# Optimization experiments

Measured on AMD Instinct MI355X. Metric: run time of the kernel, lower is better.

## Reference

```python
import jax, jax.numpy as jnp
import numpy as np

N_NODES = 100000
N_EDGES = 640000
D = 128
L = 3


def setup_inputs() -> dict:
    key = jax.random.key(0)
    k1, k2, k3 = jax.random.split(key, 3)
    x = jax.random.normal(k1, (N_NODES, D), dtype=jnp.float32)
    edge_index = jax.random.randint(k2, (2, N_EDGES), 0, N_NODES, dtype=jnp.int64)
    batch = jnp.zeros((N_NODES,), dtype=jnp.int64)
    W = jax.random.normal(k3, (L, D, D), dtype=jnp.float32) / np.sqrt(D)
    b = jnp.zeros((L, D), dtype=jnp.float32)
    return {"x": x, "edge_index": edge_index, "batch": batch, "W": W, "b": b}


def _gcn_forward(x, edge_index, W, b):
    row, col = edge_index[0], edge_index[1]  # source, target
    n = x.shape[0]
    # symmetric normalization (PyG gcn_norm, add_self_loops=False, unit edge weights)
    deg = jax.ops.segment_sum(jnp.ones((row.shape[0],), dtype=x.dtype), col, num_segments=n)
    dinv = jnp.where(deg > 0, jax.lax.rsqrt(jnp.where(deg > 0, deg, 1.0)), 0.0)
    norm = dinv[row] * dinv[col]  # [E]
    for i in range(W.shape[0]):
        h = x @ W[i]                                   # [N, D]
        msg = h[row] * norm[:, None]                   # gather + scale, [E, D]
        x = jax.ops.segment_sum(msg, col, num_segments=n) + b[i]
        if i < W.shape[0] - 1:
            x = jax.nn.relu(x)
    return x


def reference(x, edge_index, batch, W, b):
    return _gcn_forward(x, edge_index, W, b)
```

## Files before the change

kernel.cpp:

```cpp
#include <hip/hip_runtime.h>
#include <hip/hip_fp16.h>
#include <math.h>

#define NN 100000
#define NE 640000
#define DD 128
#define LSTRIDE 132
#define SLOT_CAP 32

typedef __attribute__((ext_vector_type(8))) short short8;
typedef __attribute__((ext_vector_type(4))) float floatx4;

#define EPI_PRE_F32 0
#define EPI_PRE_F16 1
#define EPI_FINAL   2

static const size_t OFF_DEG    = 0;
static const size_t OFF_GCTR   = 400000;
static const size_t OFF_DINV   = 400064;
static const size_t OFF_OFF    = 800064;
static const size_t OFF_CURSOR = 1200064;
static const size_t OFF_WHP    = 1600064;
static const size_t OFF_WLP    = 1698368;
static const size_t OFF_EIDX   = 1796672;
static const size_t OFF_H_FB   = 4357120;
static const size_t WS_NEED_FB = 4357120 + (size_t)NN * DD * 4;
static const size_t OFF_SLOT   = 1796672;
static const size_t OFF_X16    = 14596672;
static const size_t OFF_ZA     = 40196928;
static const size_t WS_NEED_SL = 40196928 + (size_t)(NN + 1) * DD * 2;

__device__ __forceinline__ unsigned bf16_rne(float f) {
    unsigned u = __float_as_uint(f);
    return (u + 0x7FFFu + ((u >> 16) & 1u)) >> 16;
}

__device__ __forceinline__ void pack_W(int t, const float* __restrict__ W,
                                       ushort* __restrict__ Whp,
                                       ushort* __restrict__ Wlp) {
    if (t < 3 * 2048) {
        int l = t >> 11;
        int r = t & 2047;
        int kc = r >> 9;
        int nt = (r >> 6) & 7;
        int L  = r & 63;
        int n  = nt * 16 + (L & 15);
        int k0 = kc * 32 + (L >> 4) * 8;
        const float* Wl_ = W + (size_t)l * DD * DD;
        size_t base = ((size_t)l * 2048 + r) * 8;
        #pragma unroll
        for (int j = 0; j < 8; ++j) {
            float f = Wl_[(size_t)(k0 + j) * DD + n];
            unsigned hi = bf16_rne(f);
            float fh = __uint_as_float(hi << 16);
            unsigned lo = bf16_rne(f - fh);
            Whp[base + j] = (ushort)hi;
            Wlp[base + j] = (ushort)lo;
        }
    }
}

__global__ __launch_bounds__(256) void fill_slots_pack(const int* __restrict__ rowi,
                                                       const int* __restrict__ coli,
                                                       int* __restrict__ cnt,
                                                       int* __restrict__ slot,
                                                       const float* __restrict__ W,
                                                       ushort* __restrict__ Whp,
                                                       ushort* __restrict__ Wlp) {
    int t = blockIdx.x * 256 + threadIdx.x;
    int e0 = t * 4;
    if (e0 < NE) {
        int4 s4 = *(const int4*)(rowi + e0);
        int4 d4 = *(const int4*)(coli + e0);
        int p0 = atomicAdd(&cnt[d4.x], 1);
        int p1 = atomicAdd(&cnt[d4.y], 1);
        int p2 = atomicAdd(&cnt[d4.z], 1);
        int p3 = atomicAdd(&cnt[d4.w], 1);
        if (p0 < SLOT_CAP) slot[(d4.x << 5) + p0] = s4.x;
        if (p1 < SLOT_CAP) slot[(d4.y << 5) + p1] = s4.y;
        if (p2 < SLOT_CAP) slot[(d4.z << 5) + p2] = s4.z;
        if (p3 < SLOT_CAP) slot[(d4.w << 5) + p3] = s4.w;
    }
    pack_W(t, W, Whp, Wlp);
}

__global__ __launch_bounds__(256) void prescale_convert(const float* __restrict__ x,
                                                        int* __restrict__ cnt,
                                                        float* __restrict__ dinv,
                                                        __half* __restrict__ x16,
                                                        __half* __restrict__ za) {
    int t = blockIdx.x * 256 + threadIdx.x;
    int row = t >> 5;
    int c4  = (t & 31) * 4;
    int d = cnt[row];
    float s = (d > 0) ? 1.0f / sqrtf((float)d) : 0.0f;
    if ((t & 31) == 0) {
        if (d > SLOT_CAP) cnt[row] = SLOT_CAP;
        dinv[row] = s;
    }
    float4 v = *(const float4*)(x + (size_t)row * DD + c4);
    __half2 p0 = __floats2half2_rn(v.x * s, v.y * s);
    __half2 p1 = __floats2half2_rn(v.z * s, v.w * s);
    uint2 w;
    w.x = *(unsigned*)&p0;
    w.y = *(unsigned*)&p1;
    *(uint2*)(x16 + (size_t)row * DD + c4) = w;
    if (blockIdx.x == 0 && threadIdx.x < 128) {
        __half z = __float2half(0.f);
        x16[(size_t)NN * DD + threadIdx.x] = z;
        za [(size_t)NN * DD + threadIdx.x] = z;
    }
}

__global__ __launch_bounds__(256) void count_and_pack(const int* __restrict__ coli,
                                                      int* __restrict__ deg,
                                                      const float* __restrict__ W,
                                                      ushort* __restrict__ Whp,
                                                      ushort* __restrict__ Wlp) {
    int e = blockIdx.x * 256 + threadIdx.x;
    if (e < NE) atomicAdd(&deg[coli[e]], 1);
    pack_W(e, W, Whp, Wlp);
}

__global__ __launch_bounds__(256) void alloc_offsets(const int* __restrict__ deg,
                                                     int* __restrict__ off,
                                                     int* __restrict__ cursor,
                                                     float* __restrict__ dinv,
                                                     unsigned* __restrict__ gctr) {
    int i = blockIdx.x * 256 + threadIdx.x;
    int v = (i < NN) ? deg[i] : 0;
    if (i < NN) dinv[i] = (v > 0) ? 1.0f / sqrtf((float)v) : 0.0f;

    int lane = threadIdx.x & 63;
    int sv = v;
    #pragma unroll
    for (int s = 1; s < 64; s <<= 1) {
        int t = __shfl_up(sv, s, 64);
        if (lane >= s) sv += t;
    }
    int wtot = __shfl(sv, 63, 64);
    int base = 0;
    if (lane == 63) base = (int)atomicAdd(gctr, (unsigned)wtot);
    base = __shfl(base, 63, 64);
    int o = base + sv - v;
    if (i < NN) {
        off[i] = o;
        cursor[i] = o;
    }
}

__global__ __launch_bounds__(256) void fill_csr(const int* __restrict__ rowi,
                                                const int* __restrict__ coli,
                                                int* __restrict__ cursor,
                                                int* __restrict__ eidx) {
    int e = blockIdx.x * 256 + threadIdx.x;
    if (e < NE) {
        int s = rowi[e], d = coli[e];
        int pos = atomicAdd(&cursor[d], 1);
        eidx[pos] = s;
    }
}

template<int EPI>
__device__ __forceinline__ void mfma_phase(const float* __restrict__ Ls,
                                           const ushort* __restrict__ Whp,
                                           const ushort* __restrict__ Wlp,
                                           const float* __restrict__ dinv,
                                           const float* __restrict__ bias,
                                           void* __restrict__ Yout,
                                           int n0, int tid) {
    int wave = tid >> 6;
    int lane = tid & 63;
    int m    = lane & 15;
    int quad = lane >> 4;
    int mt   = wave >> 1;
    int nh   = (wave & 1) * 4;

    floatx4 acc[4];
    #pragma unroll
    for (int q = 0; q < 4; ++q) acc[q] = (floatx4){0.f, 0.f, 0.f, 0.f};

    #pragma unroll
    for (int kc = 0; kc < 4; ++kc) {
        const float* lp = &Ls[(mt * 16 + m) * LSTRIDE + kc * 32 + quad * 8];
        float4 xa = *(const float4*)(lp);
        float4 xb = *(const float4*)(lp + 4);
        float xs[8] = {xa.x, xa.y, xa.z, xa.w, xb.x, xb.y, xb.z, xb.w};
        short8 ah, al;
        #pragma unroll
        for (int j = 0; j < 8; ++j) {
            unsigned hi = bf16_rne(xs[j]);
            float fh = __uint_as_float(hi << 16);
            unsigned lo = bf16_rne(xs[j] - fh);
            ah[j] = (short)hi;
            al[j] = (short)lo;
        }
        #pragma unroll
        for (int q = 0; q < 4; ++q) {
            int nt = nh + q;
            size_t fidx = (((size_t)(kc * 8 + nt)) * 64 + lane) * 8;
            short8 bh = *(const short8*)(Whp + fidx);
            short8 bl = *(const short8*)(Wlp + fidx);
            acc[q] = __builtin_amdgcn_mfma_f32_16x16x32_bf16(al, bh, acc[q], 0, 0, 0);
            acc[q] = __builtin_amdgcn_mfma_f32_16x16x32_bf16(ah, bl, acc[q], 0, 0, 0);
            acc[q] = __builtin_amdgcn_mfma_f32_16x16x32_bf16(ah, bh, acc[q], 0, 0, 0);
        }
    }

    #pragma unroll
    for (int i = 0; i < 4; ++i) {
        int ro = n0 + mt * 16 + quad * 4 + i;
        float s = dinv[ro];
        float s2 = s * s;
        #pragma unroll
        for (int q = 0; q < 4; ++q) {
            int col = (nh + q) * 16 + m;
            if (EPI == EPI_FINAL) {
                float v = fmaf(acc[q][i], s, bias[col]);
                ((float*)Yout)[(size_t)ro * DD + col] = v;
            } else {
                float v = fmaf(acc[q][i], s2, bias[col] * s);
                v = fmaxf(v, 0.f);
                if (EPI == EPI_PRE_F32)
                    ((float*)Yout)[(size_t)ro * DD + col] = v;
                else
                    ((__half*)Yout)[(size_t)ro * DD + col] = __float2half(v);
            }
        }
    }
}

template<int EPI>
__global__ __launch_bounds__(256) void fused_layer_f16(
        const __half* __restrict__ Xin,
        const ushort* __restrict__ Whp,
        const ushort* __restrict__ Wlp,
        const int* __restrict__ deg,
        const int* __restrict__ slot,
        const float* __restrict__ dinv,
        const float* __restrict__ bias,
        void* __restrict__ Yout) {
    __shared__ float Ls[32 * LSTRIDE];
    int tid  = threadIdx.x;
    int n0   = blockIdx.x * 32;
    int wave = tid >> 6, lane = tid & 63;

    int nbase = n0 + wave * 8;
    int4 srow = *(const int4*)(slot + (size_t)nbase * 32 + lane * 4);
    int  d8   = deg[nbase + (lane & 7)];

    #pragma unroll 1
    for (int nl = 0; nl < 8; ++nl) {
        int d = __shfl(d8, nl, 64);
        float2 acc = make_float2(0.f, 0.f);
        for (int j0 = 0; j0 < d; j0 += 8) {
            int rem = d - j0;
            int idx[8];
            #pragma unroll
            for (int k = 0; k < 8; ++k) {
                int owner = nl * 8 + (j0 >> 2) + (k >> 2);
                int e;
                switch (k & 3) {
                    case 0:  e = srow.x; break;
                    case 1:  e = srow.y; break;
                    case 2:  e = srow.z; break;
                    default: e = srow.w; break;
                }
                e = __shfl(e, owner, 64);
                idx[k] = (k < rem) ? e : NN;
            }
            __half2 v[8];
            #pragma unroll
            for (int k = 0; k < 8; ++k)
                v[k] = *(const __half2*)(Xin + (size_t)idx[k] * DD + lane * 2);
            #pragma unroll
            for (int k = 0; k < 8; ++k) {
                float2 f = __half22float2(v[k]);
                acc.x += f.x;
                acc.y += f.y;
            }
        }
        *(float2*)(&Ls[(wave * 8 + nl) * LSTRIDE + lane * 2]) = acc;
    }
    __syncthreads();

    mfma_phase<EPI>(Ls, Whp, Wlp, dinv, bias, Yout, n0, tid);
}

template<int GMODE, int EPI>
__global__ __launch_bounds__(256) void fused_layer_csr(
        const float* __restrict__ Xin,
        const ushort* __restrict__ Whp,
        const ushort* __restrict__ Wlp,
        const int* __restrict__ off,
        const int* __restrict__ deg,
        const int* __restrict__ eidx,
        const float* __restrict__ dinv,
        const float* __restrict__ bias,
        void* __restrict__ Yout) {
    __shared__ float Ls[32 * LSTRIDE];
    int tid = threadIdx.x;
    int n0 = blockIdx.x * 32;
    {
        int g = tid >> 5, lane = tid & 31;
        int c0 = lane * 4;
        #pragma unroll
        for (int t = 0; t < 4; ++t) {
            int nl = g * 4 + t;
            int node = n0 + nl;
            float4 a0 = make_float4(0.f, 0.f, 0.f, 0.f);
            float4 a1 = a0, a2 = a0, a3 = a0;
            {
                int s = off[node];
                int e = s + deg[node];
                for (int j = s; j < e; j += 4) {
                    int j1 = j + 1, j2 = j + 2, j3 = j + 3;
                    int i1 = (j1 < e) ? j1 : j;
                    int i2 = (j2 < e) ? j2 : j;
                    int i3 = (j3 < e) ? j3 : j;
                    int s0 = eidx[j],  s1 = eidx[i1];
                    int s2 = eidx[i2], s3 = eidx[i3];
                    float w0, w1, w2, w3;
                    if (GMODE == 0) {
                        w0 = dinv[s0];
                        w1 = (j1 < e) ? dinv[s1] : 0.f;
                        w2 = (j2 < e) ? dinv[s2] : 0.f;
                        w3 = (j3 < e) ? dinv[s3] : 0.f;
                    } else {
                        w0 = 1.f;
                        w1 = (j1 < e) ? 1.f : 0.f;
                        w2 = (j2 < e) ? 1.f : 0.f;
                        w3 = (j3 < e) ? 1.f : 0.f;
                    }
                    float4 v0 = *(const float4*)(Xin + (size_t)s0 * DD + c0);
                    float4 v1 = *(const float4*)(Xin + (size_t)s1 * DD + c0);
                    float4 v2 = *(const float4*)(Xin + (size_t)s2 * DD + c0);
                    float4 v3 = *(const float4*)(Xin + (size_t)s3 * DD + c0);
                    a0.x = fmaf(w0, v0.x, a0.x); a0.y = fmaf(w0, v0.y, a0.y);
                    a0.z = fmaf(w0, v0.z, a0.z); a0.w = fmaf(w0, v0.w, a0.w);
                    a1.x = fmaf(w1, v1.x, a1.x); a1.y = fmaf(w1, v1.y, a1.y);
                    a1.z = fmaf(w1, v1.z, a1.z); a1.w = fmaf(w1, v1.w, a1.w);
                    a2.x = fmaf(w2, v2.x, a2.x); a2.y = fmaf(w2, v2.y, a2.y);
                    a2.z = fmaf(w2, v2.z, a2.z); a2.w = fmaf(w2, v2.w, a2.w);
                    a3.x = fmaf(w3, v3.x, a3.x); a3.y = fmaf(w3, v3.y, a3.y);
                    a3.z = fmaf(w3, v3.z, a3.z); a3.w = fmaf(w3, v3.w, a3.w);
                }
            }
            float4 r = make_float4((a0.x + a1.x) + (a2.x + a3.x),
                                   (a0.y + a1.y) + (a2.y + a3.y),
                                   (a0.z + a1.z) + (a2.z + a3.z),
                                   (a0.w + a1.w) + (a2.w + a3.w));
            *(float4*)(&Ls[nl * LSTRIDE + c0]) = r;
        }
    }
    __syncthreads();
    mfma_phase<EPI>(Ls, Whp, Wlp, dinv, bias, Yout, n0, tid);
}


extern "C" void kernel_launch(void* const* d_in, const int* in_sizes, int n_in,
                              void* d_out, int out_size, void* d_ws, size_t ws_size,
                              hipStream_t stream) {
    const float* x  = (const float*)d_in[0];
    const int*   ei = (const int*)d_in[1];
    const float* W  = (const float*)d_in[3];
    const float* b  = (const float*)d_in[4];
    float* out = (float*)d_out;

    char* ws = (char*)d_ws;
    int*      deg    = (int*)(ws + OFF_DEG);
    unsigned* gctr   = (unsigned*)(ws + OFF_GCTR);
    float*    dinv   = (float*)(ws + OFF_DINV);
    int*      off    = (int*)(ws + OFF_OFF);
    int*      cursor = (int*)(ws + OFF_CURSOR);
    ushort*   whp    = (ushort*)(ws + OFF_WHP);
    ushort*   wlp    = (ushort*)(ws + OFF_WLP);

    const int* rowi = ei;
    const int* coli = ei + NE;

    int nblk = NN / 32;

    if (ws_size >= WS_NEED_SL) {
        int*    slot = (int*)(ws + OFF_SLOT);
        __half* x16  = (__half*)(ws + OFF_X16);
        __half* za   = (__half*)(ws + OFF_ZA);
        __half* zb   = x16;

        hipMemsetAsync(ws + OFF_DEG, 0, 400000, stream);
        fill_slots_pack<<<NE / 4 / 256, 256, 0, stream>>>(rowi, coli, deg, slot,
                                                          W, whp, wlp);
        prescale_convert<<<NN * 32 / 256, 256, 0, stream>>>(x, deg, dinv, x16, za);

        fused_layer_f16<EPI_PRE_F16><<<nblk, 256, 0, stream>>>(x16, whp,         wlp,
                                                               deg, slot, dinv, b,          za);
        fused_layer_f16<EPI_PRE_F16><<<nblk, 256, 0, stream>>>(za,  whp + 16384, wlp + 16384,
                                                               deg, slot, dinv, b + DD,     zb);
        fused_layer_f16<EPI_FINAL  ><<<nblk, 256, 0, stream>>>(zb,  whp + 32768, wlp + 32768,
                                                               deg, slot, dinv, b + 2 * DD, out);
    } else {
        int*   eidx = (int*)(ws + OFF_EIDX);
        float* H    = (float*)(ws + OFF_H_FB);
        hipMemsetAsync(ws, 0, 400064, stream);
        count_and_pack<<<(NE + 255) / 256, 256, 0, stream>>>(coli, deg, W, whp, wlp);
        alloc_offsets<<<(NN + 255) / 256, 256, 0, stream>>>(deg, off, cursor, dinv, gctr);
        fill_csr<<<(NE + 255) / 256, 256, 0, stream>>>(rowi, coli, cursor, eidx);

        fused_layer_csr<0, EPI_PRE_F32><<<nblk, 256, 0, stream>>>(x,   whp,         wlp,
                                                                  off, deg, eidx, dinv, b,          out);
        fused_layer_csr<1, EPI_PRE_F32><<<nblk, 256, 0, stream>>>(out, whp + 16384, wlp + 16384,
                                                                  off, deg, eidx, dinv, b + DD,     H);
        fused_layer_csr<1, EPI_FINAL  ><<<nblk, 256, 0, stream>>>(H,   whp + 32768, wlp + 32768,
                                                                  off, deg, eidx, dinv, b + 2 * DD, out);
    }
}
```

Measured before the change: 290.3 us.

## Fuse x fp16 conversion into slot fill and weight first-layer gather by dinv

Folds the fp32-to-fp16 conversion of x into the slot-filling kernel, which no longer needs the degree, and moves the degree clamp and dinv computation into a small per-node kernel. Because x is no longer prescaled by dinv, the first layer's gather loads dinv for each neighbour and uses FMA-weighted accumulation. This drops a full pass over x that depended on degrees, at the cost of extra dinv gathers in layer one and one atomic per thread instead of four batched ones. dinv[NN] is set to zero so padded indices contribute nothing, which assumes the dinv buffer has room for that extra entry.

```diff
diff --git a/kernel.cpp b/kernel.cpp
--- a/kernel.cpp
+++ b/kernel.cpp
@@ -60,51 +60,49 @@
     }
 }
 
-__global__ __launch_bounds__(256) void fill_slots_pack(const int* __restrict__ rowi,
-                                                       const int* __restrict__ coli,
-                                                       int* __restrict__ cnt,
-                                                       int* __restrict__ slot,
-                                                       const float* __restrict__ W,
-                                                       ushort* __restrict__ Whp,
-                                                       ushort* __restrict__ Wlp) {
+__global__ __launch_bounds__(256) void fuse_setup(const int* __restrict__ rowi,
+                                                  const int* __restrict__ coli,
+                                                  int* __restrict__ cnt,
+                                                  int* __restrict__ slot,
+                                                  const float* __restrict__ W,
+                                                  ushort* __restrict__ Whp,
+                                                  ushort* __restrict__ Wlp,
+                                                  const float* __restrict__ x,
+                                                  __half* __restrict__ x16) {
     int t = blockIdx.x * 256 + threadIdx.x;
-    int e0 = t * 4;
-    if (e0 < NE) {
-        int4 s4 = *(const int4*)(rowi + e0);
-        int4 d4 = *(const int4*)(coli + e0);
-        int p0 = atomicAdd(&cnt[d4.x], 1);
-        int p1 = atomicAdd(&cnt[d4.y], 1);
-        int p2 = atomicAdd(&cnt[d4.z], 1);
-        int p3 = atomicAdd(&cnt[d4.w], 1);
-        if (p0 < SLOT_CAP) slot[(d4.x << 5) + p0] = s4.x;
-        if (p1 < SLOT_CAP) slot[(d4.y << 5) + p1] = s4.y;
-        if (p2 < SLOT_CAP) slot[(d4.z << 5) + p2] = s4.z;
-        if (p3 < SLOT_CAP) slot[(d4.w << 5) + p3] = s4.w;
+    if (t < NE) {
+        int s = rowi[t], d = coli[t];
+        int p = atomicAdd(&cnt[d], 1);
+        if (p < SLOT_CAP) slot[(d << 5) + p] = s;
     }
     pack_W(t, W, Whp, Wlp);
-}
-
-__global__ __launch_bounds__(256) void prescale_convert(const float* __restrict__ x,
-                                                        int* __restrict__ cnt,
-                                                        float* __restrict__ dinv,
-                                                        __half* __restrict__ x16,
-                                                        __half* __restrict__ za) {
-    int t = blockIdx.x * 256 + threadIdx.x;
-    int row = t >> 5;
-    int c4  = (t & 31) * 4;
-    int d = cnt[row];
-    float s = (d > 0) ? 1.0f / sqrtf((float)d) : 0.0f;
-    if ((t & 31) == 0) {
-        if (d > SLOT_CAP) cnt[row] = SLOT_CAP;
-        dinv[row] = s;
-    }
-    float4 v = *(const float4*)(x + (size_t)row * DD + c4);
-    __half2 p0 = __floats2half2_rn(v.x * s, v.y * s);
-    __half2 p1 = __floats2half2_rn(v.z * s, v.w * s);
-    uint2 w;
-    w.x = *(unsigned*)&p0;
-    w.y = *(unsigned*)&p1;
-    *(uint2*)(x16 + (size_t)row * DD + c4) = w;
+    {
+        int row = t >> 4;
+        int c8  = (t & 15) * 8;
+        float4 va = *(const float4*)(x + (size_t)row * DD + c8);
+        float4 vb = *(const float4*)(x + (size_t)row * DD + c8 + 4);
+        __half2 h0 = __floats2half2_rn(va.x, va.y);
+        __half2 h1 = __floats2half2_rn(va.z, va.w);
+        __half2 h2 = __floats2half2_rn(vb.x, vb.y);
+        __half2 h3 = __floats2half2_rn(vb.z, vb.w);
+        uint4 w4;
+        w4.x = *(unsigned*)&h0; w4.y = *(unsigned*)&h1;
+        w4.z = *(unsigned*)&h2; w4.w = *(unsigned*)&h3;
+        *(uint4*)(x16 + (size_t)row * DD + c8) = w4;
+    }
+}
+
+__global__ __launch_bounds__(256) void finish_setup(int* __restrict__ cnt,
+                                                    float* __restrict__ dinv,
+                                                    __half* __restrict__ x16,
+                                                    __half* __restrict__ za) {
+    int i = blockIdx.x * 256 + threadIdx.x;
+    if (i < NN) {
+        int d = cnt[i];
+        if (d > SLOT_CAP) { d = SLOT_CAP; cnt[i] = d; }
+        dinv[i] = (d > 0) ? 1.0f / sqrtf((float)d) : 0.0f;
+    }
+    if (i == NN) dinv[NN] = 0.0f;
     if (blockIdx.x == 0 && threadIdx.x < 128) {
         __half z = __float2half(0.f);
         x16[(size_t)NN * DD + threadIdx.x] = z;
@@ -230,7 +228,7 @@
     }
 }
 
-template<int EPI>
+template<int EPI, bool WEIGHTED>
 __global__ __launch_bounds__(256) void fused_layer_f16(
         const __half* __restrict__ Xin,
         const ushort* __restrict__ Whp,
@@ -269,6 +267,11 @@
                 e = __shfl(e, owner, 64);
                 idx[k] = (k < rem) ? e : NN;
             }
+            float wgt[8];
+            if (WEIGHTED) {
+                #pragma unroll
+                for (int k = 0; k < 8; ++k) wgt[k] = dinv[idx[k]];
+            }
             __half2 v[8];
             #pragma unroll
             for (int k = 0; k < 8; ++k)
@@ -276,8 +279,13 @@
             #pragma unroll
             for (int k = 0; k < 8; ++k) {
                 float2 f = __half22float2(v[k]);
-                acc.x += f.x;
-                acc.y += f.y;
+                if (WEIGHTED) {
+                    acc.x = fmaf(wgt[k], f.x, acc.x);
+                    acc.y = fmaf(wgt[k], f.y, acc.y);
+                } else {
+                    acc.x += f.x;
+                    acc.y += f.y;
+                }
             }
         }
         *(float2*)(&Ls[(wave * 8 + nl) * LSTRIDE + lane * 2]) = acc;
@@ -388,16 +396,16 @@
         __half* zb   = x16;
 
         hipMemsetAsync(ws + OFF_DEG, 0, 400000, stream);
-        fill_slots_pack<<<NE / 4 / 256, 256, 0, stream>>>(rowi, coli, deg, slot,
-                                                          W, whp, wlp);
-        prescale_convert<<<NN * 32 / 256, 256, 0, stream>>>(x, deg, dinv, x16, za);
-
-        fused_layer_f16<EPI_PRE_F16><<<nblk, 256, 0, stream>>>(x16, whp,         wlp,
-                                                               deg, slot, dinv, b,          za);
-        fused_layer_f16<EPI_PRE_F16><<<nblk, 256, 0, stream>>>(za,  whp + 16384, wlp + 16384,
-                                                               deg, slot, dinv, b + DD,     zb);
-        fused_layer_f16<EPI_FINAL  ><<<nblk, 256, 0, stream>>>(zb,  whp + 32768, wlp + 32768,
-                                                               deg, slot, dinv, b + 2 * DD, out);
+        fuse_setup<<<NN * DD / 8 / 256, 256, 0, stream>>>(rowi, coli, deg, slot,
+                                                          W, whp, wlp, x, x16);
+        finish_setup<<<(NN + 256) / 256, 256, 0, stream>>>(deg, dinv, x16, za);
+
+        fused_layer_f16<EPI_PRE_F16, true ><<<nblk, 256, 0, stream>>>(x16, whp,         wlp,
+                                                                      deg, slot, dinv, b,          za);
+        fused_layer_f16<EPI_PRE_F16, false><<<nblk, 256, 0, stream>>>(za,  whp + 16384, wlp + 16384,
+                                                                      deg, slot, dinv, b + DD,     zb);
+        fused_layer_f16<EPI_FINAL,   false><<<nblk, 256, 0, stream>>>(zb,  whp + 32768, wlp + 32768,
+                                                                      deg, slot, dinv, b + 2 * DD, out);
     } else {
         int*   eidx = (int*)(ws + OFF_EIDX);
         float* H    = (float*)(ws + OFF_H_FB);
```

Measured after the change: 292.3 us. Within noise of the previous version (+0.7%).
